# Performance work log

Measured on AMD Instinct MI355X. Metric: run time of the kernel, lower is better.

Reference implementation:

```python
import jax, jax.numpy as jnp
import numpy as np

D = 768
H = 12
MLP = 3072
EPS = 1e-5


def _layernorm(x, g, b):
    mu = jnp.mean(x, axis=-1, keepdims=True)
    var = jnp.var(x, axis=-1, keepdims=True)
    return (x - mu) * jax.lax.rsqrt(var + EPS) * g + b


def setup_inputs() -> dict:
    key = jax.random.key(0)
    ks = jax.random.split(key, 16)
    s = 0.02
    inp = {
        "x": jax.random.normal(ks[0], (8, 1024, D), dtype=jnp.float32),
        "ln1_g": jnp.ones((D,), jnp.float32),
        "ln1_b": jnp.zeros((D,), jnp.float32),
        "Wq": jax.random.normal(ks[1], (D, D), jnp.float32) * s,
        "bq": jnp.zeros((D,), jnp.float32),
        "Wk": jax.random.normal(ks[2], (D, D), jnp.float32) * s,
        "bk": jnp.zeros((D,), jnp.float32),
        "Wv": jax.random.normal(ks[3], (D, D), jnp.float32) * s,
        "bv": jnp.zeros((D,), jnp.float32),
        "Wo": jax.random.normal(ks[4], (D, D), jnp.float32) * s,
        "bo": jnp.zeros((D,), jnp.float32),
        "ln2_g": jnp.ones((D,), jnp.float32),
        "ln2_b": jnp.zeros((D,), jnp.float32),
        "W1": jax.random.normal(ks[5], (D, MLP), jnp.float32) * s,
        "b1": jnp.zeros((MLP,), jnp.float32),
        "W2": jax.random.normal(ks[6], (MLP, D), jnp.float32) * s,
        "b2": jnp.zeros((D,), jnp.float32),
    }
    return inp


def reference(x, ln1_g, ln1_b, Wq, bq, Wk, bk, Wv, bv, Wo, bo, ln2_g, ln2_b, W1, b1, W2, b2):
    b, n, d = x.shape
    dh = d // H
    scale = 1.0 / jnp.sqrt(jnp.float32(d))  # NOTE: sqrt(input_dim), per source

    h = _layernorm(x, ln1_g, ln1_b)
    q = (h @ Wq + bq).reshape(b, n, H, dh).transpose(0, 2, 1, 3)  # bhnf
    k = (h @ Wk + bk).reshape(b, n, H, dh).transpose(0, 2, 1, 3)
    v = (h @ Wv + bv).reshape(b, n, H, dh).transpose(0, 2, 1, 3)

    score = jax.nn.softmax(jnp.einsum('bhif,bhjf->bhij', q, k) * scale, axis=-1)
    attn = jnp.einsum('bhij,bhjf->bihf', score, v).reshape(b, n, d)
    out = attn @ Wo + bo + x  # residual (dropout p=0)

    h2 = _layernorm(out, ln2_g, ln2_b)
    mlp = jax.nn.gelu(jax.nn.gelu(h2 @ W1 + b1, approximate=False) @ W2 + b2, approximate=False)
    return mlp + out
```

## Files before the change

### kernel.cpp

```cpp
#include <hip/hip_runtime.h>
#include <hip/hip_bf16.h>
#include <math.h>

typedef __bf16 bf16x8 __attribute__((ext_vector_type(8)));
typedef float f32x4 __attribute__((ext_vector_type(4)));

#define DD 768
#define HH 12
#define MLPD 3072
#define QSCALE 0.036084391824351615f

__device__ __forceinline__ float gelu_fast(float x) {
    float y = 1.5957691216057308f * x + 0.07135481283154893f * x * x * x;
    return x * __builtin_amdgcn_rcpf(1.0f + __expf(-y));
}

__device__ __forceinline__ void gload16(const void* g, void* l) {
    __builtin_amdgcn_global_load_lds(
        (const __attribute__((address_space(1))) unsigned int*)g,
        (__attribute__((address_space(3))) unsigned int*)l, 16, 0, 0);
}

__device__ __forceinline__ void hard_barrier() {
    __builtin_amdgcn_sched_barrier(0);
    __builtin_amdgcn_s_barrier();
    __builtin_amdgcn_sched_barrier(0);
}

__device__ __forceinline__ void ln_row(const float* __restrict__ xr,
                                       const float* __restrict__ g,
                                       const float* __restrict__ b,
                                       __bf16* __restrict__ orow, int lane) {
    float4 v[3];
    float s = 0.f, ss = 0.f;
#pragma unroll
    for (int i = 0; i < 3; ++i) {
        v[i] = *reinterpret_cast<const float4*>(&xr[(i * 64 + lane) * 4]);
        s += v[i].x + v[i].y + v[i].z + v[i].w;
        ss += v[i].x * v[i].x + v[i].y * v[i].y + v[i].z * v[i].z + v[i].w * v[i].w;
    }
#pragma unroll
    for (int m = 1; m < 64; m <<= 1) {
        s += __shfl_xor(s, m);
        ss += __shfl_xor(ss, m);
    }
    float mu = s * (1.0f / DD);
    float rstd = rsqrtf(ss * (1.0f / DD) - mu * mu + 1e-5f);
#pragma unroll
    for (int i = 0; i < 3; ++i) {
        int c = (i * 64 + lane) * 4;
        float4 gv = *reinterpret_cast<const float4*>(&g[c]);
        float4 bv = *reinterpret_cast<const float4*>(&b[c]);
        union { __bf16 h[4]; uint2 u; } o;
        o.h[0] = (__bf16)((v[i].x - mu) * rstd * gv.x + bv.x);
        o.h[1] = (__bf16)((v[i].y - mu) * rstd * gv.y + bv.y);
        o.h[2] = (__bf16)((v[i].z - mu) * rstd * gv.z + bv.z);
        o.h[3] = (__bf16)((v[i].w - mu) * rstd * gv.w + bv.w);
        *reinterpret_cast<uint2*>(&orow[c]) = o.u;
    }
}

__global__ __launch_bounds__(256) void ln_kernel(const float* __restrict__ X,
                                                 const float* __restrict__ g,
                                                 const float* __restrict__ b,
                                                 __bf16* __restrict__ O) {
    int row = blockIdx.x * 4 + (threadIdx.x >> 6);
    ln_row(X + (size_t)row * DD, g, b, O + (size_t)row * DD, threadIdx.x & 63);
}

__global__ __launch_bounds__(256) void prep_kernel(
    const float* __restrict__ Wq, const float* __restrict__ Wk,
    const float* __restrict__ Wv, const float* __restrict__ Wo,
    const float* __restrict__ W1, const float* __restrict__ W2,
    __bf16* __restrict__ wqkv, __bf16* __restrict__ wo,
    __bf16* __restrict__ w1, __bf16* __restrict__ w2,
    const float* __restrict__ x, const float* __restrict__ ln1_g,
    const float* __restrict__ ln1_b, __bf16* __restrict__ h) {
    __shared__ float tile[64][65];
    int blk = blockIdx.x;
    if (blk >= 1728) {
        int row = (blk - 1728) * 4 + (threadIdx.x >> 6);
        ln_row(x + (size_t)row * DD, ln1_g, ln1_b, h + (size_t)row * DD, threadIdx.x & 63);
        return;
    }
    const float* W; __bf16* Wt; int K, N, tk, tn;
    if (blk < 432) {
        int wsel = blk / 144, r = blk - wsel * 144;
        W = wsel == 0 ? Wq : (wsel == 1 ? Wk : Wv);
        Wt = wqkv + (size_t)wsel * 768 * 768;
        K = 768; N = 768; tk = r % 12; tn = r / 12;
    } else if (blk < 576) {
        int r = blk - 432; W = Wo; Wt = wo; K = 768; N = 768; tk = r % 12; tn = r / 12;
    } else if (blk < 1152) {
        int r = blk - 576; W = W1; Wt = w1; K = 768; N = 3072; tk = r % 12; tn = r / 12;
    } else {
        int r = blk - 1152; W = W2; Wt = w2; K = 3072; N = 768; tk = r % 48; tn = r / 48;
    }
    int k0 = tk * 64, n0 = tn * 64;
    int t = threadIdx.x;
    int tr = t >> 6, tc = t & 63;
#pragma unroll
    for (int i = 0; i < 16; ++i) {
        int row = i * 4 + tr;
        tile[row][tc] = W[(size_t)(k0 + row) * N + n0 + tc];
    }
    __syncthreads();
#pragma unroll
    for (int i = 0; i < 16; ++i) {
        int row = i * 4 + tr;
        Wt[(size_t)(n0 + row) * K + k0 + tc] = (__bf16)tile[tc][row];
    }
}

template <int EPI>
__global__ __launch_bounds__(512, 4) void gemm_pl(
    const __bf16* __restrict__ A, const __bf16* __restrict__ Bt,
    const float* __restrict__ b0, const float* __restrict__ b1, const float* __restrict__ b2,
    void* __restrict__ o0, void* __restrict__ o1, void* __restrict__ o2,
    const float* __restrict__ resid, int M, int N, int K) {
    extern __shared__ __bf16 lds[];
    __bf16* As = lds;
    __bf16* Bs = lds + 16384;
    const int t = threadIdx.x;
    const int w = t >> 6, lane = t & 63;
    const int wm = w >> 2, wn = w & 3;
    const int lr = lane & 15, lg = lane >> 4;
    const int m0 = blockIdx.x * 128, n0 = blockIdx.y * 128;
    const int lrow8 = lane >> 3;
    const int cSwz = ((lane & 7) ^ lrow8) * 8;

    const __bf16* aSrc = A + (size_t)(m0 + w * 16 + lrow8) * K + cSwz;
    const __bf16* bSrc = Bt + (size_t)(n0 + w * 16 + lrow8) * K + cSwz;
    const int ldsW = w * 16 * 64;

    const int nt = K >> 6;
    f32x4 acc[4][2] = {};

    auto stage = [&](int T) {
        const int buf = (T & 1) * 8192;
#pragma unroll
        for (int c = 0; c < 2; ++c)
            gload16(aSrc + (size_t)(c * 8) * K + T * 64, &As[buf + ldsW + c * 8 * 64]);
#pragma unroll
        for (int c = 0; c < 2; ++c)
            gload16(bSrc + (size_t)(c * 8) * K + T * 64, &Bs[buf + ldsW + c * 8 * 64]);
    };

    stage(0);
    for (int T = 0; T < nt; ++T) {
        if (T + 1 < nt) {
            stage(T + 1);
            asm volatile("s_waitcnt vmcnt(4)" ::: "memory");
        } else {
            asm volatile("s_waitcnt vmcnt(0)" ::: "memory");
        }
        hard_barrier();
        const int buf = (T & 1) * 8192;
#pragma unroll
        for (int kg = 0; kg < 2; ++kg) {
            bf16x8 af[4], bfr[2];
#pragma unroll
            for (int i = 0; i < 4; ++i)
                af[i] = *reinterpret_cast<const bf16x8*>(
                    &As[buf + (wm * 64 + i * 16 + lr) * 64 + (((kg << 2) | lg) ^ (lr & 7)) * 8]);
#pragma unroll
            for (int j = 0; j < 2; ++j)
                bfr[j] = *reinterpret_cast<const bf16x8*>(
                    &Bs[buf + (wn * 32 + j * 16 + lr) * 64 + (((kg << 2) | lg) ^ (lr & 7)) * 8]);
#pragma unroll
            for (int i = 0; i < 4; ++i)
#pragma unroll
                for (int j = 0; j < 2; ++j)
                    acc[i][j] = __builtin_amdgcn_mfma_f32_16x16x32_bf16(bfr[j], af[i], acc[i][j], 0, 0, 0);
        }
        hard_barrier();
    }

#pragma unroll
    for (int i = 0; i < 4; ++i) {
        const int m = m0 + wm * 64 + i * 16 + lr;
        const int bI = m >> 10, ntok = m & 1023;
#pragma unroll
        for (int j = 0; j < 2; ++j) {
            const int n = n0 + wn * 32 + j * 16 + lg * 4;
            if (EPI == 0) {
                const int wid = n / 768;
                const int cc0 = n - wid * 768;
                const int hh = cc0 >> 6, f0 = cc0 & 63;
                const float* bsel = (wid == 0 ? b0 : (wid == 1 ? b1 : b2));
                const float4 bv = *reinterpret_cast<const float4*>(&bsel[cc0]);
                const float v0 = acc[i][j][0] + bv.x, v1 = acc[i][j][1] + bv.y;
                const float v2 = acc[i][j][2] + bv.z, v3 = acc[i][j][3] + bv.w;
                if (wid == 0) {
                    union { __bf16 h[4]; uint2 u; } pk;
                    pk.h[0] = (__bf16)(v0 * QSCALE); pk.h[1] = (__bf16)(v1 * QSCALE);
                    pk.h[2] = (__bf16)(v2 * QSCALE); pk.h[3] = (__bf16)(v3 * QSCALE);
                    *reinterpret_cast<uint2*>(
                        &((__bf16*)o0)[((((size_t)(bI * HH + hh) << 10) + ntok) << 6) + f0]) = pk.u;
                } else if (wid == 1) {
                    union { __bf16 h[4]; uint2 u; } pk;
                    pk.h[0] = (__bf16)v0; pk.h[1] = (__bf16)v1;
                    pk.h[2] = (__bf16)v2; pk.h[3] = (__bf16)v3;
                    *reinterpret_cast<uint2*>(
                        &((__bf16*)o1)[((((size_t)(bI * HH + hh) << 10) + ntok) << 6) + f0]) = pk.u;
                } else {
                    __bf16* vb = (__bf16*)o2;
                    size_t base = ((size_t)(bI * HH + hh) * 64 + f0) << 10;
                    vb[base + ntok] = (__bf16)v0;
                    vb[base + (1 << 10) + ntok] = (__bf16)v1;
                    vb[base + (2 << 10) + ntok] = (__bf16)v2;
                    vb[base + (3 << 10) + ntok] = (__bf16)v3;
                }
            } else if (EPI == 3) {
                const float4 bv = *reinterpret_cast<const float4*>(&b0[n]);
                union { __bf16 h[4]; uint2 u; } pk;
                pk.h[0] = (__bf16)gelu_fast(acc[i][j][0] + bv.x);
                pk.h[1] = (__bf16)gelu_fast(acc[i][j][1] + bv.y);
                pk.h[2] = (__bf16)gelu_fast(acc[i][j][2] + bv.z);
                pk.h[3] = (__bf16)gelu_fast(acc[i][j][3] + bv.w);
                *reinterpret_cast<uint2*>(&((__bf16*)o0)[(size_t)m * MLPD + n]) = pk.u;
            } else {
                const float4 bv = *reinterpret_cast<const float4*>(&b0[n]);
                const float v0 = acc[i][j][0] + bv.x, v1 = acc[i][j][1] + bv.y;
                const float v2 = acc[i][j][2] + bv.z, v3 = acc[i][j][3] + bv.w;
                const float4 rv = *reinterpret_cast<const float4*>(&resid[(size_t)m * DD + n]);
                if (EPI == 2) {
                    float4 ov = {v0 + rv.x, v1 + rv.y, v2 + rv.z, v3 + rv.w};
                    *reinterpret_cast<float4*>(&((float*)o0)[(size_t)m * DD + n]) = ov;
                } else {
                    float4 ov = {gelu_fast(v0) + rv.x, gelu_fast(v1) + rv.y,
                                 gelu_fast(v2) + rv.z, gelu_fast(v3) + rv.w};
                    *reinterpret_cast<float4*>(&((float*)o0)[(size_t)m * DD + n]) = ov;
                }
            }
        }
    }
}

__global__ __launch_bounds__(512, 6) void attn_kernel(
    const __bf16* __restrict__ Q, const __bf16* __restrict__ Kg,
    const __bf16* __restrict__ Vt, __bf16* __restrict__ Aout) {
    __shared__ char KsB[2][64 * 128];
    __shared__ char VsB[2][64 * 128];
    __shared__ char PsB[8][16 * 128];
    const int id = blockIdx.x;
    const int swz = (id & 7) * 96 + (id >> 3);
    const int bh = swz >> 3, qt = swz & 7;
    const int t = threadIdx.x, w = t >> 6, lane = t & 63;
    const int lr = lane & 15, lg = lane >> 4;
    const size_t bhN = (size_t)bh << 10;
    const int q0 = qt * 128;

    bf16x8 qf[2];
#pragma unroll
    for (int kg = 0; kg < 2; ++kg)
        qf[kg] = *reinterpret_cast<const bf16x8*>(&Q[(bhN + q0 + w * 16 + lr) * 64 + kg * 32 + lg * 8]);

    const int srow = t >> 3;
    const int sc = ((t & 7) ^ (srow & 7)) * 16;
    const char* kbase = (const char*)Kg + bhN * 128;
    const char* vbase = (const char*)Vt + ((size_t)bh << 17);
    const int wlds = w * 1024;

    f32x4 oacc[4] = {};
    float lsum[4] = {0.f, 0.f, 0.f, 0.f};

    gload16(kbase + (size_t)srow * 128 + sc, KsB[0] + wlds);
    gload16(vbase + (size_t)srow * 2048 + sc, VsB[0] + wlds);

    for (int kt = 0; kt < 16; ++kt) {
        const int buf = kt & 1;
        if (kt < 15) {
            gload16(kbase + (size_t)((kt + 1) * 64 + srow) * 128 + sc, KsB[buf ^ 1] + wlds);
            gload16(vbase + (size_t)srow * 2048 + (kt + 1) * 128 + sc, VsB[buf ^ 1] + wlds);
            asm volatile("s_waitcnt vmcnt(2)" ::: "memory");
        } else {
            asm volatile("s_waitcnt vmcnt(0)" ::: "memory");
        }
        __builtin_amdgcn_sched_barrier(0);
        __builtin_amdgcn_s_barrier();
        __builtin_amdgcn_sched_barrier(0);

        f32x4 s[4] = {};
        __builtin_amdgcn_s_setprio(1);
#pragma unroll
        for (int kg = 0; kg < 2; ++kg) {
#pragma unroll
            for (int j = 0; j < 4; ++j) {
                int row = j * 16 + lr;
                bf16x8 kf = *reinterpret_cast<const bf16x8*>(
                    KsB[buf] + ((row * 128 + kg * 64 + lg * 16) ^ ((row & 7) << 4)));
                s[j] = __builtin_amdgcn_mfma_f32_16x16x32_bf16(qf[kg], kf, s[j], 0, 0, 0);
            }
        }
        __builtin_amdgcn_s_setprio(0);

#pragma unroll
        for (int r = 0; r < 4; ++r) {
            int prow = lg * 4 + r;
#pragma unroll
            for (int j = 0; j < 2; ++j) {
                float pv = __expf(s[j][r]);
                lsum[r] += pv;
                *reinterpret_cast<__bf16*>(
                    PsB[w] + ((prow * 128 + (j * 16 + lr) * 2) ^ ((prow & 7) << 4))) = (__bf16)pv;
            }
        }
        bf16x8 pf0 = *reinterpret_cast<const bf16x8*>(
            PsB[w] + ((lr * 128 + 0 * 64 + lg * 16) ^ ((lr & 7) << 4)));
#pragma unroll
        for (int r = 0; r < 4; ++r) {
            int prow = lg * 4 + r;
#pragma unroll
            for (int j = 2; j < 4; ++j) {
                float pv = __expf(s[j][r]);
                lsum[r] += pv;
                *reinterpret_cast<__bf16*>(
                    PsB[w] + ((prow * 128 + (j * 16 + lr) * 2) ^ ((prow & 7) << 4))) = (__bf16)pv;
            }
        }
#pragma unroll
        for (int j = 0; j < 4; ++j) {
            int row = j * 16 + lr;
            bf16x8 vf = *reinterpret_cast<const bf16x8*>(
                VsB[buf] + ((row * 128 + 0 * 64 + lg * 16) ^ ((row & 7) << 4)));
            oacc[j] = __builtin_amdgcn_mfma_f32_16x16x32_bf16(pf0, vf, oacc[j], 0, 0, 0);
        }
        bf16x8 pf1 = *reinterpret_cast<const bf16x8*>(
            PsB[w] + ((lr * 128 + 1 * 64 + lg * 16) ^ ((lr & 7) << 4)));
#pragma unroll
        for (int j = 0; j < 4; ++j) {
            int row = j * 16 + lr;
            bf16x8 vf = *reinterpret_cast<const bf16x8*>(
                VsB[buf] + ((row * 128 + 1 * 64 + lg * 16) ^ ((row & 7) << 4)));
            oacc[j] = __builtin_amdgcn_mfma_f32_16x16x32_bf16(pf1, vf, oacc[j], 0, 0, 0);
        }
        __builtin_amdgcn_sched_barrier(0);
        __builtin_amdgcn_s_barrier();
        __builtin_amdgcn_sched_barrier(0);
    }

#pragma unroll
    for (int r = 0; r < 4; ++r)
#pragma unroll
        for (int m = 1; m < 16; m <<= 1) lsum[r] += __shfl_xor(lsum[r], m);

    const int bI = bh / HH, hh = bh % HH;
#pragma unroll
    for (int r = 0; r < 4; ++r) {
        float inv = 1.0f / lsum[r];
        int qrow = q0 + w * 16 + lg * 4 + r;
        size_t base = ((size_t)(bI << 10) + qrow) * DD + hh * 64;
#pragma unroll
        for (int j = 0; j < 4; ++j)
            Aout[base + j * 16 + lr] = (__bf16)(oacc[j][r] * inv);
    }
}

extern "C" void kernel_launch(void* const* d_in, const int* in_sizes, int n_in,
                              void* d_out, int out_size, void* d_ws, size_t ws_size,
                              hipStream_t stream) {
    const float* x     = (const float*)d_in[0];
    const float* ln1_g = (const float*)d_in[1];
    const float* ln1_b = (const float*)d_in[2];
    const float* Wq    = (const float*)d_in[3];
    const float* bq    = (const float*)d_in[4];
    const float* Wk    = (const float*)d_in[5];
    const float* bk    = (const float*)d_in[6];
    const float* Wv    = (const float*)d_in[7];
    const float* bv    = (const float*)d_in[8];
    const float* Wo    = (const float*)d_in[9];
    const float* bo    = (const float*)d_in[10];
    const float* ln2_g = (const float*)d_in[11];
    const float* ln2_b = (const float*)d_in[12];
    const float* W1    = (const float*)d_in[13];
    const float* b1    = (const float*)d_in[14];
    const float* W2    = (const float*)d_in[15];
    const float* b2    = (const float*)d_in[16];

    char* p = (char*)d_ws;
    auto alloc = [&](size_t bytes) { char* r = p; p += bytes; return r; };
    __bf16* wqkv_t = (__bf16*)alloc((size_t)2304 * 768 * 2);
    __bf16* wo_t   = (__bf16*)alloc((size_t)768 * 768 * 2);
    __bf16* w1_t   = (__bf16*)alloc((size_t)3072 * 768 * 2);
    __bf16* w2_t   = (__bf16*)alloc((size_t)768 * 3072 * 2);
    __bf16* h      = (__bf16*)alloc((size_t)8192 * 768 * 2);
    float*  outb   = (float*) alloc((size_t)8192 * 768 * 4);
    __bf16* q      = (__bf16*)alloc((size_t)8192 * 768 * 2);
    __bf16* kb     = (__bf16*)alloc((size_t)8192 * 768 * 2);
    __bf16* vt     = (__bf16*)alloc((size_t)8192 * 768 * 2);
    __bf16* attn   = (__bf16*)alloc((size_t)8192 * 768 * 2);
    __bf16* mid    = q;

    const int LDSP = 65536;
    hipFuncSetAttribute(reinterpret_cast<const void*>(gemm_pl<0>),
                        hipFuncAttributeMaxDynamicSharedMemorySize, LDSP);
    hipFuncSetAttribute(reinterpret_cast<const void*>(gemm_pl<2>),
                        hipFuncAttributeMaxDynamicSharedMemorySize, LDSP);
    hipFuncSetAttribute(reinterpret_cast<const void*>(gemm_pl<3>),
                        hipFuncAttributeMaxDynamicSharedMemorySize, LDSP);
    hipFuncSetAttribute(reinterpret_cast<const void*>(gemm_pl<4>),
                        hipFuncAttributeMaxDynamicSharedMemorySize, LDSP);

    prep_kernel<<<3776, 256, 0, stream>>>(Wq, Wk, Wv, Wo, W1, W2,
                                          wqkv_t, wo_t, w1_t, w2_t,
                                          x, ln1_g, ln1_b, h);
    gemm_pl<0><<<dim3(64, 18), 512, LDSP, stream>>>(h, wqkv_t, bq, bk, bv, q, kb, vt,
                                                    nullptr, 8192, 2304, 768);
    attn_kernel<<<768, 512, 0, stream>>>(q, kb, vt, attn);
    gemm_pl<2><<<dim3(64, 6), 512, LDSP, stream>>>(attn, wo_t, bo, nullptr, nullptr, outb,
                                                   nullptr, nullptr, x, 8192, 768, 768);
    ln_kernel<<<2048, 256, 0, stream>>>(outb, ln2_g, ln2_b, h);
    gemm_pl<3><<<dim3(64, 24), 512, LDSP, stream>>>(h, w1_t, b1, nullptr, nullptr, mid,
                                                    nullptr, nullptr, nullptr, 8192, 3072, 768);
    gemm_pl<4><<<dim3(64, 6), 512, LDSP, stream>>>(mid, w2_t, b2, nullptr, nullptr, (float*)d_out,
                                                   nullptr, nullptr, outb, 8192, 768, 3072);
}
```

Before: 226.4 us.

## Use 256x128 tile GEMM with 4 waves for QKV and MLP-up projections

Adds a gemm_big kernel with 256-thread blocks, each wave computing a 128x64 output sub-tile (8x4 MFMA accumulators), and uses it for the QKV and W1 GEMMs. The larger per-wave tile raises MFMA work per LDS fragment load and halves the number of blocks. The trade-off is higher register pressure, 96KB LDS per block, and fewer blocks in flight (576 and 768 blocks) to hide latency. The Wo and W2 GEMMs keep the original kernel, whose signature is trimmed; the attention barriers are replaced by the equivalent hard_barrier helper.

```diff
diff --git a/kernel.cpp b/kernel.cpp
--- a/kernel.cpp
+++ b/kernel.cpp
@@ -113,76 +113,84 @@
 }
 
 template <int EPI>
-__global__ __launch_bounds__(512, 4) void gemm_pl(
+__global__ __launch_bounds__(256, 1) void gemm_big(
     const __bf16* __restrict__ A, const __bf16* __restrict__ Bt,
     const float* __restrict__ b0, const float* __restrict__ b1, const float* __restrict__ b2,
     void* __restrict__ o0, void* __restrict__ o1, void* __restrict__ o2,
-    const float* __restrict__ resid, int M, int N, int K) {
+    int M, int N, int K) {
     extern __shared__ __bf16 lds[];
-    __bf16* As = lds;
-    __bf16* Bs = lds + 16384;
     const int t = threadIdx.x;
     const int w = t >> 6, lane = t & 63;
-    const int wm = w >> 2, wn = w & 3;
+    const int wm = w >> 1, wn = w & 1;
     const int lr = lane & 15, lg = lane >> 4;
-    const int m0 = blockIdx.x * 128, n0 = blockIdx.y * 128;
+    const int m0 = blockIdx.x * 256, n0 = blockIdx.y * 128;
     const int lrow8 = lane >> 3;
     const int cSwz = ((lane & 7) ^ lrow8) * 8;
 
-    const __bf16* aSrc = A + (size_t)(m0 + w * 16 + lrow8) * K + cSwz;
-    const __bf16* bSrc = Bt + (size_t)(n0 + w * 16 + lrow8) * K + cSwz;
-    const int ldsW = w * 16 * 64;
+    const __bf16* usrc[12];
+    int ulds[12], utog[12];
+#pragma unroll
+    for (int c = 0; c < 12; ++c) {
+        int u = w * 12 + c;
+        if (u < 32) {
+            usrc[c] = A + (size_t)(m0 + u * 8 + lrow8) * K + cSwz;
+            ulds[c] = u * 512;
+            utog[c] = 16384;
+        } else {
+            usrc[c] = Bt + (size_t)(n0 + (u - 32) * 8 + lrow8) * K + cSwz;
+            ulds[c] = 32768 + (u - 32) * 512;
+            utog[c] = 8192;
+        }
+    }
 
     const int nt = K >> 6;
-    f32x4 acc[4][2] = {};
+    f32x4 acc[8][4] = {};
 
     auto stage = [&](int T) {
-        const int buf = (T & 1) * 8192;
-#pragma unroll
-        for (int c = 0; c < 2; ++c)
-            gload16(aSrc + (size_t)(c * 8) * K + T * 64, &As[buf + ldsW + c * 8 * 64]);
-#pragma unroll
-        for (int c = 0; c < 2; ++c)
-            gload16(bSrc + (size_t)(c * 8) * K + T * 64, &Bs[buf + ldsW + c * 8 * 64]);
+        const int tb = (T & 1);
+#pragma unroll
+        for (int c = 0; c < 12; ++c)
+            gload16(usrc[c] + (size_t)T * 64, &lds[ulds[c] + tb * utog[c]]);
     };
 
     stage(0);
     for (int T = 0; T < nt; ++T) {
         if (T + 1 < nt) {
             stage(T + 1);
-            asm volatile("s_waitcnt vmcnt(4)" ::: "memory");
+            asm volatile("s_waitcnt vmcnt(12)" ::: "memory");
         } else {
             asm volatile("s_waitcnt vmcnt(0)" ::: "memory");
         }
         hard_barrier();
-        const int buf = (T & 1) * 8192;
+        const int bufA = (T & 1) * 16384, bufB = 32768 + (T & 1) * 8192;
 #pragma unroll
         for (int kg = 0; kg < 2; ++kg) {
-            bf16x8 af[4], bfr[2];
-#pragma unroll
-            for (int i = 0; i < 4; ++i)
+            const int chunk = (((kg << 2) | lg) ^ (lr & 7)) * 8;
+            bf16x8 af[8], bfr[4];
+#pragma unroll
+            for (int i = 0; i < 8; ++i)
                 af[i] = *reinterpret_cast<const bf16x8*>(
-                    &As[buf + (wm * 64 + i * 16 + lr) * 64 + (((kg << 2) | lg) ^ (lr & 7)) * 8]);
-#pragma unroll
-            for (int j = 0; j < 2; ++j)
+                    &lds[bufA + (wm * 128 + i * 16 + lr) * 64 + chunk]);
+#pragma unroll
+            for (int j = 0; j < 4; ++j)
                 bfr[j] = *reinterpret_cast<const bf16x8*>(
-                    &Bs[buf + (wn * 32 + j * 16 + lr) * 64 + (((kg << 2) | lg) ^ (lr & 7)) * 8]);
-#pragma unroll
-            for (int i = 0; i < 4; ++i)
-#pragma unroll
-                for (int j = 0; j < 2; ++j)
+                    &lds[bufB + (wn * 64 + j * 16 + lr) * 64 + chunk]);
+#pragma unroll
+            for (int i = 0; i < 8; ++i)
+#pragma unroll
+                for (int j = 0; j < 4; ++j)
                     acc[i][j] = __builtin_amdgcn_mfma_f32_16x16x32_bf16(bfr[j], af[i], acc[i][j], 0, 0, 0);
         }
         hard_barrier();
     }
 
 #pragma unroll
-    for (int i = 0; i < 4; ++i) {
-        const int m = m0 + wm * 64 + i * 16 + lr;
+    for (int i = 0; i < 8; ++i) {
+        const int m = m0 + wm * 128 + i * 16 + lr;
         const int bI = m >> 10, ntok = m & 1023;
 #pragma unroll
-        for (int j = 0; j < 2; ++j) {
-            const int n = n0 + wn * 32 + j * 16 + lg * 4;
+        for (int j = 0; j < 4; ++j) {
+            const int n = n0 + wn * 64 + j * 16 + lg * 4;
             if (EPI == 0) {
                 const int wid = n / 768;
                 const int cc0 = n - wid * 768;
@@ -211,7 +219,7 @@
                     vb[base + (2 << 10) + ntok] = (__bf16)v2;
                     vb[base + (3 << 10) + ntok] = (__bf16)v3;
                 }
-            } else if (EPI == 3) {
+            } else {
                 const float4 bv = *reinterpret_cast<const float4*>(&b0[n]);
                 union { __bf16 h[4]; uint2 u; } pk;
                 pk.h[0] = (__bf16)gelu_fast(acc[i][j][0] + bv.x);
@@ -219,19 +227,91 @@
                 pk.h[2] = (__bf16)gelu_fast(acc[i][j][2] + bv.z);
                 pk.h[3] = (__bf16)gelu_fast(acc[i][j][3] + bv.w);
                 *reinterpret_cast<uint2*>(&((__bf16*)o0)[(size_t)m * MLPD + n]) = pk.u;
+            }
+        }
+    }
+}
+
+template <int EPI>
+__global__ __launch_bounds__(512, 4) void gemm_pl(
+    const __bf16* __restrict__ A, const __bf16* __restrict__ Bt,
+    const float* __restrict__ b0, void* __restrict__ o0,
+    const float* __restrict__ resid, int M, int N, int K) {
+    extern __shared__ __bf16 lds[];
+    __bf16* As = lds;
+    __bf16* Bs = lds + 16384;
+    const int t = threadIdx.x;
+    const int w = t >> 6, lane = t & 63;
+    const int wm = w >> 2, wn = w & 3;
+    const int lr = lane & 15, lg = lane >> 4;
+    const int m0 = blockIdx.x * 128, n0 = blockIdx.y * 128;
+    const int lrow8 = lane >> 3;
+    const int cSwz = ((lane & 7) ^ lrow8) * 8;
+
+    const __bf16* aSrc = A + (size_t)(m0 + w * 16 + lrow8) * K + cSwz;
+    const __bf16* bSrc = Bt + (size_t)(n0 + w * 16 + lrow8) * K + cSwz;
+    const int ldsW = w * 16 * 64;
+
+    const int nt = K >> 6;
+    f32x4 acc[4][2] = {};
+
+    auto stage = [&](int T) {
+        const int buf = (T & 1) * 8192;
+#pragma unroll
+        for (int c = 0; c < 2; ++c)
+            gload16(aSrc + (size_t)(c * 8) * K + T * 64, &As[buf + ldsW + c * 8 * 64]);
+#pragma unroll
+        for (int c = 0; c < 2; ++c)
+            gload16(bSrc + (size_t)(c * 8) * K + T * 64, &Bs[buf + ldsW + c * 8 * 64]);
+    };
+
+    stage(0);
+    for (int T = 0; T < nt; ++T) {
+        if (T + 1 < nt) {
+            stage(T + 1);
+            asm volatile("s_waitcnt vmcnt(4)" ::: "memory");
+        } else {
+            asm volatile("s_waitcnt vmcnt(0)" ::: "memory");
+        }
+        hard_barrier();
+        const int buf = (T & 1) * 8192;
+#pragma unroll
+        for (int kg = 0; kg < 2; ++kg) {
+            bf16x8 af[4], bfr[2];
+#pragma unroll
+            for (int i = 0; i < 4; ++i)
+                af[i] = *reinterpret_cast<const bf16x8*>(
+                    &As[buf + (wm * 64 + i * 16 + lr) * 64 + (((kg << 2) | lg) ^ (lr & 7)) * 8]);
+#pragma unroll
+            for (int j = 0; j < 2; ++j)
+                bfr[j] = *reinterpret_cast<const bf16x8*>(
+                    &Bs[buf + (wn * 32 + j * 16 + lr) * 64 + (((kg << 2) | lg) ^ (lr & 7)) * 8]);
+#pragma unroll
+            for (int i = 0; i < 4; ++i)
+#pragma unroll
+                for (int j = 0; j < 2; ++j)
+                    acc[i][j] = __builtin_amdgcn_mfma_f32_16x16x32_bf16(bfr[j], af[i], acc[i][j], 0, 0, 0);
+        }
+        hard_barrier();
+    }
+
+#pragma unroll
+    for (int i = 0; i < 4; ++i) {
+        const int m = m0 + wm * 64 + i * 16 + lr;
+#pragma unroll
+        for (int j = 0; j < 2; ++j) {
+            const int n = n0 + wn * 32 + j * 16 + lg * 4;
+            const float4 bv = *reinterpret_cast<const float4*>(&b0[n]);
+            const float v0 = acc[i][j][0] + bv.x, v1 = acc[i][j][1] + bv.y;
+            const float v2 = acc[i][j][2] + bv.z, v3 = acc[i][j][3] + bv.w;
+            const float4 rv = *reinterpret_cast<const float4*>(&resid[(size_t)m * DD + n]);
+            if (EPI == 2) {
+                float4 ov = {v0 + rv.x, v1 + rv.y, v2 + rv.z, v3 + rv.w};
+                *reinterpret_cast<float4*>(&((float*)o0)[(size_t)m * DD + n]) = ov;
             } else {
-                const float4 bv = *reinterpret_cast<const float4*>(&b0[n]);
-                const float v0 = acc[i][j][0] + bv.x, v1 = acc[i][j][1] + bv.y;
-                const float v2 = acc[i][j][2] + bv.z, v3 = acc[i][j][3] + bv.w;
-                const float4 rv = *reinterpret_cast<const float4*>(&resid[(size_t)m * DD + n]);
-                if (EPI == 2) {
-                    float4 ov = {v0 + rv.x, v1 + rv.y, v2 + rv.z, v3 + rv.w};
-                    *reinterpret_cast<float4*>(&((float*)o0)[(size_t)m * DD + n]) = ov;
-                } else {
-                    float4 ov = {gelu_fast(v0) + rv.x, gelu_fast(v1) + rv.y,
-                                 gelu_fast(v2) + rv.z, gelu_fast(v3) + rv.w};
-                    *reinterpret_cast<float4*>(&((float*)o0)[(size_t)m * DD + n]) = ov;
-                }
+                float4 ov = {gelu_fast(v0) + rv.x, gelu_fast(v1) + rv.y,
+                             gelu_fast(v2) + rv.z, gelu_fast(v3) + rv.w};
+                *reinterpret_cast<float4*>(&((float*)o0)[(size_t)m * DD + n]) = ov;
             }
         }
     }
@@ -277,9 +357,7 @@
         } else {
             asm volatile("s_waitcnt vmcnt(0)" ::: "memory");
         }
-        __builtin_amdgcn_sched_barrier(0);
-        __builtin_amdgcn_s_barrier();
-        __builtin_amdgcn_sched_barrier(0);
+        hard_barrier();
 
         f32x4 s[4] = {};
         __builtin_amdgcn_s_setprio(1);
@@ -335,9 +413,7 @@
                 VsB[buf] + ((row * 128 + 1 * 64 + lg * 16) ^ ((row & 7) << 4)));
             oacc[j] = __builtin_amdgcn_mfma_f32_16x16x32_bf16(pf1, vf, oacc[j], 0, 0, 0);
         }
-        __builtin_amdgcn_sched_barrier(0);
-        __builtin_amdgcn_s_barrier();
-        __builtin_amdgcn_sched_barrier(0);
+        hard_barrier();
     }
 
 #pragma unroll
@@ -392,12 +468,13 @@
     __bf16* attn   = (__bf16*)alloc((size_t)8192 * 768 * 2);
     __bf16* mid    = q;
 
+    const int LDSB = 98304;
     const int LDSP = 65536;
-    hipFuncSetAttribute(reinterpret_cast<const void*>(gemm_pl<0>),
-                        hipFuncAttributeMaxDynamicSharedMemorySize, LDSP);
+    hipFuncSetAttribute(reinterpret_cast<const void*>(gemm_big<0>),
+                        hipFuncAttributeMaxDynamicSharedMemorySize, LDSB);
+    hipFuncSetAttribute(reinterpret_cast<const void*>(gemm_big<3>),
+                        hipFuncAttributeMaxDynamicSharedMemorySize, LDSB);
     hipFuncSetAttribute(reinterpret_cast<const void*>(gemm_pl<2>),
-                        hipFuncAttributeMaxDynamicSharedMemorySize, LDSP);
-    hipFuncSetAttribute(reinterpret_cast<const void*>(gemm_pl<3>),
                         hipFuncAttributeMaxDynamicSharedMemorySize, LDSP);
     hipFuncSetAttribute(reinterpret_cast<const void*>(gemm_pl<4>),
                         hipFuncAttributeMaxDynamicSharedMemorySize, LDSP);
@@ -405,14 +482,13 @@
     prep_kernel<<<3776, 256, 0, stream>>>(Wq, Wk, Wv, Wo, W1, W2,
                                           wqkv_t, wo_t, w1_t, w2_t,
                                           x, ln1_g, ln1_b, h);
-    gemm_pl<0><<<dim3(64, 18), 512, LDSP, stream>>>(h, wqkv_t, bq, bk, bv, q, kb, vt,
-                                                    nullptr, 8192, 2304, 768);
+    gemm_big<0><<<dim3(32, 18), 256, LDSB, stream>>>(h, wqkv_t, bq, bk, bv, q, kb, vt,
+                                                     8192, 2304, 768);
     attn_kernel<<<768, 512, 0, stream>>>(q, kb, vt, attn);
-    gemm_pl<2><<<dim3(64, 6), 512, LDSP, stream>>>(attn, wo_t, bo, nullptr, nullptr, outb,
-                                                   nullptr, nullptr, x, 8192, 768, 768);
+    gemm_pl<2><<<dim3(64, 6), 512, LDSP, stream>>>(attn, wo_t, bo, outb, x, 8192, 768, 768);
     ln_kernel<<<2048, 256, 0, stream>>>(outb, ln2_g, ln2_b, h);
-    gemm_pl<3><<<dim3(64, 24), 512, LDSP, stream>>>(h, w1_t, b1, nullptr, nullptr, mid,
-                                                    nullptr, nullptr, nullptr, 8192, 3072, 768);
-    gemm_pl<4><<<dim3(64, 6), 512, LDSP, stream>>>(mid, w2_t, b2, nullptr, nullptr, (float*)d_out,
-                                                   nullptr, nullptr, outb, 8192, 768, 3072);
-}
+    gemm_big<3><<<dim3(32, 24), 256, LDSB, stream>>>(h, w1_t, b1, nullptr, nullptr, mid,
+                                                     nullptr, nullptr, 8192, 3072, 768);
+    gemm_pl<4><<<dim3(64, 6), 512, LDSP, stream>>>(mid, w2_t, b2, (float*)d_out, outb,
+                                                   8192, 768, 3072);
+}
```

Result: slower. 259.5 us (+14.6%).
